# Kernel optimization log

Measured on AMD Instinct MI355X. Metric: run time of the kernel, lower is better.

Reference implementation:

```python
import jax, jax.numpy as jnp
import numpy as np

N = 100000      # nodes
E = 1600000     # edges (avg degree 16)
F_IN = 48       # input features
H = 64          # hidden
C = 2           # classes


def _init(key, shape, fan_in):
    return jax.random.normal(key, shape, jnp.float32) * (1.0 / np.sqrt(fan_in))


def setup_inputs() -> dict:
    key = jax.random.key(0)
    ks = jax.random.split(key, 12)
    return {
        "x": jax.random.normal(ks[0], (N, F_IN), jnp.float32),
        "edge_index": jax.random.randint(ks[1], (2, E), 0, N, dtype=jnp.int64),
        "W1l": _init(ks[2], (F_IN, H), F_IN),
        "b1l": jnp.zeros((H,), jnp.float32),
        "W1r": _init(ks[3], (F_IN, H), F_IN),
        "W2l": _init(ks[4], (H, H), H),
        "b2l": jnp.zeros((H,), jnp.float32),
        "W2r": _init(ks[5], (H, H), H),
        "Wlin1": _init(ks[6], (H, H), H),
        "blin1": jnp.zeros((H,), jnp.float32),
        "Wlin2": _init(ks[7], (H, C), H),
        "blin2": jnp.zeros((C,), jnp.float32),
    }


def _sage_conv(x, src, dst, Wl, bl, Wr, num_nodes):
    # mean aggregation of source-node features onto destination nodes
    msg = x[src]                                              # [E, F] gather
    agg = jax.ops.segment_sum(msg, dst, num_segments=num_nodes)
    cnt = jax.ops.segment_sum(jnp.ones((dst.shape[0], 1), x.dtype), dst,
                              num_segments=num_nodes)
    mean = agg / jnp.maximum(cnt, 1.0)
    # PyG SAGEConv: lin_l(aggr) + lin_r(root); bias only on lin_l
    return mean @ Wl + bl + x @ Wr


def reference(x, edge_index, W1l, b1l, W1r, W2l, b2l, W2r,
              Wlin1, blin1, Wlin2, blin2):
    src, dst = edge_index[0], edge_index[1]
    n = x.shape[0]
    h = jax.nn.sigmoid(_sage_conv(x, src, dst, W1l, b1l, W1r, n))
    h = jax.nn.sigmoid(_sage_conv(h, src, dst, W2l, b2l, W2r, n))
    # dropout(p=0.5) is identity in eval mode (self.training=False)
    h = jax.nn.sigmoid(h @ Wlin1 + blin1)
    return jax.nn.softmax(h @ Wlin2 + blin2, axis=1)
```

## Files before the change

### kernel.cpp

```cpp
#include <hip/hip_runtime.h>
#include <math.h>


#define NF1 48
#define HH 64
#define BKT_SHIFT 8
#define BKT_SZ (1 << BKT_SHIFT)
#define BCAP 4800
#define EPB 16

typedef __attribute__((ext_vector_type(8))) short short8v;
typedef __attribute__((ext_vector_type(4))) float float4v;

__device__ __forceinline__ float sigmoidf_(float v) {
  return 1.0f / (1.0f + __expf(-v));
}
__device__ __forceinline__ float bflo(unsigned w) {
  union { unsigned u; float f; } c; c.u = w << 16; return c.f;
}
__device__ __forceinline__ float bfhi(unsigned w) {
  union { unsigned u; float f; } c; c.u = w & 0xffff0000u; return c.f;
}
__device__ __forceinline__ unsigned short f2bf(float f) {
  union { float f; unsigned u; } c; c.f = f;
  unsigned r = c.u + 0x7fffu + ((c.u >> 16) & 1u);
  return (unsigned short)(r >> 16);
}

__global__ __launch_bounds__(256) void bin_edges(
    const int* __restrict__ ei, int* __restrict__ cursor,
    unsigned* __restrict__ bins, int E, int NB) {
  __shared__ int hist[512];
  __shared__ int gbase[512];
  for (int i = threadIdx.x; i < NB; i += 256) hist[i] = 0;
  __syncthreads();
  int base_e = blockIdx.x * (256 * EPB) + threadIdx.x;
  unsigned pk[EPB];
  int bk[EPB], rk[EPB];
#pragma unroll
  for (int k = 0; k < EPB; k++) {
    int e = base_e + k * 256;
    bk[k] = -1;
    if (e < E) {
      int s = ei[e], d = ei[E + e];
      int b = d >> BKT_SHIFT;
      pk[k] = ((unsigned)(d & (BKT_SZ - 1)) << 23) | (unsigned)s;
      bk[k] = b;
      rk[k] = atomicAdd(&hist[b], 1);
    }
  }
  __syncthreads();
  for (int i = threadIdx.x; i < NB; i += 256) {
    int c = hist[i];
    gbase[i] = (c > 0) ? atomicAdd(&cursor[i], c) : 0;
  }
  __syncthreads();
#pragma unroll
  for (int k = 0; k < EPB; k++) {
    if (bk[k] >= 0) {
      int pos = gbase[bk[k]] + rk[k];
      bins[(size_t)bk[k] * BCAP + pos] = pk[k];
    }
  }
}

__global__ __launch_bounds__(512) void scan_buckets(
    const int* __restrict__ cursor, int* __restrict__ base, int NB) {
  __shared__ int a[512], b[512];
  int tid = threadIdx.x;
  int v = (tid < NB) ? cursor[tid] : 0;
  a[tid] = v;
  __syncthreads();
  int* s = a;
  int* d = b;
  for (int off = 1; off < 512; off <<= 1) {
    int t = s[tid] + ((tid >= off) ? s[tid - off] : 0);
    d[tid] = t;
    __syncthreads();
    int* tmp = s; s = d; d = tmp;
  }
  if (tid < NB) base[tid] = s[tid] - v;
  if (tid == NB - 1) base[NB] = s[tid];
}

__global__ __launch_bounds__(256) void build_csr(
    const unsigned* __restrict__ bins, const int* __restrict__ cursor,
    const int* __restrict__ base,
    int* __restrict__ rp, int* __restrict__ csr, int n_nodes, int E, int NB) {
  __shared__ int hist[BKT_SZ];
  __shared__ int aa[BKT_SZ], bb[BKT_SZ];
  __shared__ int cur[BKT_SZ];
  int b = blockIdx.x;
  int tid = threadIdx.x;
  int node0 = b << BKT_SHIFT;
  int gb = base[b];
  int cnt = cursor[b];
  const unsigned* bp = bins + (size_t)b * BCAP;
  hist[tid] = 0;
  __syncthreads();
  for (int i = tid; i < cnt; i += 256) {
    atomicAdd(&hist[bp[i] >> 23], 1);
  }
  __syncthreads();
  int v = hist[tid];
  aa[tid] = v;
  __syncthreads();
  int* s = aa;
  int* d = bb;
  for (int off = 1; off < BKT_SZ; off <<= 1) {
    int t = s[tid] + ((tid >= off) ? s[tid - off] : 0);
    d[tid] = t;
    __syncthreads();
    int* tmp = s; s = d; d = tmp;
  }
  int loc = s[tid] - v;
  int node = node0 + tid;
  if (node < n_nodes) rp[node] = gb + loc;
  if (b == NB - 1 && tid == 0) rp[n_nodes] = E;
  cur[tid] = gb + loc;
  __syncthreads();
  for (int i = tid; i < cnt; i += 256) {
    unsigned p = bp[i];
    int dl = (int)(p >> 23);
    int pos = atomicAdd(&cur[dl], 1);
    csr[pos] = (int)(p & 0x7FFFFFu);
  }
}

template <int K>
__global__ __launch_bounds__(256, 4) void gemm_mfma(
    const float* __restrict__ X, const float* __restrict__ Wl,
    const float* __restrict__ Wr, const float* __restrict__ bias,
    unsigned short* __restrict__ t_out, float* __restrict__ r_out,
    int n_nodes) {
  __shared__ short sA[64][72];
  __shared__ short sWl[64][72];
  __shared__ short sWr[64][72];
  int lane = threadIdx.x & 63, wv = threadIdx.x >> 6;
  int l15 = lane & 15, kq = lane >> 4;

  for (int i = threadIdx.x; i < 64 * 64; i += 256) {
    int k = i >> 6, j = i & 63;
    short vl = 0, vr = 0;
    if (k < K) {
      vl = (short)f2bf(Wl[k * 64 + j]);
      vr = (short)f2bf(Wr[k * 64 + j]);
    }
    sWl[j][k] = vl;
    sWr[j][k] = vr;
  }
  if (K < 64) {
    constexpr int PADW = (64 - K) / 2;
    for (int i = threadIdx.x; i < 64 * PADW; i += 256) {
      int row = i / PADW, p = i % PADW;
      *(unsigned*)&sA[row][K + 2 * p] = 0u;
    }
  }
  float bcol[4];
#pragma unroll
  for (int c = 0; c < 4; c++) bcol[c] = bias[c * 16 + l15];

  for (int nbase = blockIdx.x * 64; nbase < n_nodes; nbase += gridDim.x * 64) {
    __syncthreads();
    for (int i = threadIdx.x; i < 64 * (K / 4); i += 256) {
      int row = i / (K / 4), c4 = i % (K / 4);
      int rr = nbase + row;
      if (rr >= n_nodes) rr = n_nodes - 1;
      float4 xv = ((const float4*)(X + (size_t)rr * K))[c4];
      unsigned lo = ((unsigned)f2bf(xv.y) << 16) | (unsigned)f2bf(xv.x);
      unsigned hi = ((unsigned)f2bf(xv.w) << 16) | (unsigned)f2bf(xv.z);
      uint2 pk = {lo, hi};
      *(uint2*)&sA[row][c4 * 4] = pk;
    }
    __syncthreads();

    float4v acc_t[4], acc_r[4];
#pragma unroll
    for (int c = 0; c < 4; c++) {
      acc_t[c] = (float4v){0.0f, 0.0f, 0.0f, 0.0f};
      acc_r[c] = (float4v){bcol[c], bcol[c], bcol[c], bcol[c]};
    }
#pragma unroll
    for (int s = 0; s < 2; s++) {
      short8v af = *(const short8v*)&sA[wv * 16 + l15][s * 32 + kq * 8];
#pragma unroll
      for (int c = 0; c < 4; c++) {
        short8v bl = *(const short8v*)&sWl[c * 16 + l15][s * 32 + kq * 8];
        short8v br = *(const short8v*)&sWr[c * 16 + l15][s * 32 + kq * 8];
        acc_t[c] = __builtin_amdgcn_mfma_f32_16x16x32_bf16(af, bl, acc_t[c], 0, 0, 0);
        acc_r[c] = __builtin_amdgcn_mfma_f32_16x16x32_bf16(af, br, acc_r[c], 0, 0, 0);
      }
    }

#pragma unroll
    for (int c = 0; c < 4; c++) {
      int j = c * 16 + l15;
#pragma unroll
      for (int g = 0; g < 4; g++) {
        int node = nbase + wv * 16 + kq * 4 + g;
        if (node < n_nodes) {
          t_out[(size_t)node * HH + j] = f2bf(acc_t[c][g]);
          r_out[(size_t)node * HH + j] = acc_r[c][g];
        }
      }
    }
  }
}

__global__ __launch_bounds__(256) void agg_sig(
    const unsigned short* __restrict__ t, const float* __restrict__ r,
    const int* __restrict__ rp, const int* __restrict__ csr,
    float* __restrict__ h, int n_nodes) {
  int grp = threadIdx.x >> 4;
  int q = threadIdx.x & 15;
  int node = blockIdx.x * 16 + grp;
  if (node >= n_nodes) return;
  int rs = rp[node], re = rp[node + 1];
  int deg = re - rs;
  const uint2* tb = (const uint2*)t + q;

  float a0 = 0, a1 = 0, a2 = 0, a3 = 0;
  int j = rs;
  for (; j + 7 < re; j += 8) {
    uint2 u0 = tb[(size_t)csr[j + 0] * 16];
    uint2 u1 = tb[(size_t)csr[j + 1] * 16];
    uint2 u2 = tb[(size_t)csr[j + 2] * 16];
    uint2 u3 = tb[(size_t)csr[j + 3] * 16];
    uint2 u4 = tb[(size_t)csr[j + 4] * 16];
    uint2 u5 = tb[(size_t)csr[j + 5] * 16];
    uint2 u6 = tb[(size_t)csr[j + 6] * 16];
    uint2 u7 = tb[(size_t)csr[j + 7] * 16];
    a0 += ((bflo(u0.x) + bflo(u1.x)) + (bflo(u2.x) + bflo(u3.x))) +
          ((bflo(u4.x) + bflo(u5.x)) + (bflo(u6.x) + bflo(u7.x)));
    a1 += ((bfhi(u0.x) + bfhi(u1.x)) + (bfhi(u2.x) + bfhi(u3.x))) +
          ((bfhi(u4.x) + bfhi(u5.x)) + (bfhi(u6.x) + bfhi(u7.x)));
    a2 += ((bflo(u0.y) + bflo(u1.y)) + (bflo(u2.y) + bflo(u3.y))) +
          ((bflo(u4.y) + bflo(u5.y)) + (bflo(u6.y) + bflo(u7.y)));
    a3 += ((bfhi(u0.y) + bfhi(u1.y)) + (bfhi(u2.y) + bfhi(u3.y))) +
          ((bfhi(u4.y) + bfhi(u5.y)) + (bfhi(u6.y) + bfhi(u7.y)));
  }
  if (j + 3 < re) {
    uint2 u0 = tb[(size_t)csr[j + 0] * 16];
    uint2 u1 = tb[(size_t)csr[j + 1] * 16];
    uint2 u2 = tb[(size_t)csr[j + 2] * 16];
    uint2 u3 = tb[(size_t)csr[j + 3] * 16];
    a0 += (bflo(u0.x) + bflo(u1.x)) + (bflo(u2.x) + bflo(u3.x));
    a1 += (bfhi(u0.x) + bfhi(u1.x)) + (bfhi(u2.x) + bfhi(u3.x));
    a2 += (bflo(u0.y) + bflo(u1.y)) + (bflo(u2.y) + bflo(u3.y));
    a3 += (bfhi(u0.y) + bfhi(u1.y)) + (bfhi(u2.y) + bfhi(u3.y));
    j += 4;
  }
  for (; j < re; j++) {
    uint2 u = tb[(size_t)csr[j] * 16];
    a0 += bflo(u.x);
    a1 += bfhi(u.x);
    a2 += bflo(u.y);
    a3 += bfhi(u.y);
  }

  float inv = 1.0f / fmaxf((float)deg, 1.0f);
  float4 rv = ((const float4*)(r + (size_t)node * HH))[q];
  float4 o;
  o.x = sigmoidf_(a0 * inv + rv.x);
  o.y = sigmoidf_(a1 * inv + rv.y);
  o.z = sigmoidf_(a2 * inv + rv.z);
  o.w = sigmoidf_(a3 * inv + rv.w);
  ((float4*)(h + (size_t)node * HH))[q] = o;
}

__global__ __launch_bounds__(512, 4) void head_k(
    const float* __restrict__ h2,
    const float* __restrict__ Wlin1, const float* __restrict__ blin1,
    const float* __restrict__ Wlin2, const float* __restrict__ blin2,
    float* __restrict__ out, int n_nodes) {
  __shared__ float sx[64][HH];
  __shared__ float sh3[64][HH];
  __shared__ float sw2[HH * 2];
  int wv = threadIdx.x >> 6, lane = threadIdx.x & 63;

  float w1[HH];
#pragma unroll
  for (int k = 0; k < HH; k++) w1[k] = Wlin1[k * HH + lane];
  float bv = blin1[lane];
  if (threadIdx.x < HH * 2) sw2[threadIdx.x] = Wlin2[threadIdx.x];
  float sb20 = blin2[0], sb21 = blin2[1];

  for (int nbase = blockIdx.x * 64; nbase < n_nodes; nbase += gridDim.x * 64) {
    __syncthreads();
    for (int i = threadIdx.x; i < 64 * (HH / 4); i += 512) {
      int row = i >> 4, c4 = i & 15;
      int rr = nbase + row;
      if (rr >= n_nodes) rr = n_nodes - 1;
      ((float4*)sx[row])[c4] = ((const float4*)(h2 + (size_t)rr * HH))[c4];
    }
    __syncthreads();

    float acc[8];
#pragma unroll
    for (int m = 0; m < 8; m++) acc[m] = bv;
#pragma unroll
    for (int k = 0; k < HH; k += 4) {
#pragma unroll
      for (int m = 0; m < 8; m++) {
        float4 a = *(const float4*)&sx[wv * 8 + m][k];
        acc[m] += a.x * w1[k] + a.y * w1[k + 1] + a.z * w1[k + 2] + a.w * w1[k + 3];
      }
    }
#pragma unroll
    for (int m = 0; m < 8; m++) sh3[wv * 8 + m][lane] = sigmoidf_(acc[m]);
    __syncthreads();

    int node_l = threadIdx.x >> 3;
    int sub = threadIdx.x & 7;
    float l0 = 0.0f, l1 = 0.0f;
#pragma unroll
    for (int kk = 0; kk < 8; kk++) {
      int k = sub * 8 + kk;
      float v = sh3[node_l][k];
      l0 += v * sw2[k * 2 + 0];
      l1 += v * sw2[k * 2 + 1];
    }
    l0 += __shfl_xor(l0, 1); l1 += __shfl_xor(l1, 1);
    l0 += __shfl_xor(l0, 2); l1 += __shfl_xor(l1, 2);
    l0 += __shfl_xor(l0, 4); l1 += __shfl_xor(l1, 4);
    int node = nbase + node_l;
    if (sub == 0 && node < n_nodes) {
      l0 += sb20;
      l1 += sb21;
      float mx = fmaxf(l0, l1);
      float p0 = __expf(l0 - mx), p1 = __expf(l1 - mx);
      float s = 1.0f / (p0 + p1);
      float2 o2 = {p0 * s, p1 * s};
      ((float2*)out)[node] = o2;
    }
  }
}

extern "C" void kernel_launch(void* const* d_in, const int* in_sizes, int n_in,
                              void* d_out, int out_size, void* d_ws, size_t ws_size,
                              hipStream_t stream) {
  const float* x     = (const float*)d_in[0];
  const int*   ei    = (const int*)d_in[1];
  const float* W1l   = (const float*)d_in[2];
  const float* b1l   = (const float*)d_in[3];
  const float* W1r   = (const float*)d_in[4];
  const float* W2l   = (const float*)d_in[5];
  const float* b2l   = (const float*)d_in[6];
  const float* W2r   = (const float*)d_in[7];
  const float* Wlin1 = (const float*)d_in[8];
  const float* blin1 = (const float*)d_in[9];
  const float* Wlin2 = (const float*)d_in[10];
  const float* blin2 = (const float*)d_in[11];
  float* out = (float*)d_out;

  int n = in_sizes[0] / NF1;
  int E = in_sizes[1] / 2;
  int NB = (n + BKT_SZ - 1) >> BKT_SHIFT;

  int* base   = (int*)d_ws;
  int* cursor = base + NB + 1;
  int* rp     = cursor + NB;
  int* csr    = rp + n + 1;
  size_t off = (size_t)(NB + 1 + NB + n + 1 + E) * sizeof(int);
  off = (off + 255) & ~(size_t)255;
  unsigned* bins = (unsigned*)((char*)d_ws + off);
  unsigned short* tbuf = (unsigned short*)bins;
  size_t reg = (size_t)NB * BCAP * sizeof(unsigned);
  size_t treg = (size_t)n * HH * sizeof(unsigned short);
  off += (reg > treg ? reg : treg);
  off = (off + 255) & ~(size_t)255;
  float* rbuf = (float*)((char*)d_ws + off);
  off += (size_t)n * HH * sizeof(float);
  off = (off + 255) & ~(size_t)255;
  float* hbuf = (float*)((char*)d_ws + off);

  hipMemsetAsync(cursor, 0, (size_t)NB * sizeof(int), stream);

  int abk = (E + 256 * EPB - 1) / (256 * EPB);
  bin_edges<<<abk, 256, 0, stream>>>(ei, cursor, bins, E, NB);
  scan_buckets<<<1, 512, 0, stream>>>(cursor, base, NB);
  build_csr<<<NB, 256, 0, stream>>>(bins, cursor, base, rp, csr, n, E, NB);

  int chunks = (n + 63) / 64;
  int gemmb = chunks < 1024 ? chunks : 1024;
  int aggb = (n + 15) / 16;
  int headb = (n + 63) / 64;
  if (headb > 1024) headb = 1024;

  gemm_mfma<NF1><<<gemmb, 256, 0, stream>>>(x, W1l, W1r, b1l, tbuf, rbuf, n);
  agg_sig<<<aggb, 256, 0, stream>>>(tbuf, rbuf, rp, csr, hbuf, n);

  gemm_mfma<HH><<<gemmb, 256, 0, stream>>>(hbuf, W2l, W2r, b2l, tbuf, rbuf, n);
  agg_sig<<<aggb, 256, 0, stream>>>(tbuf, rbuf, rp, csr, hbuf, n);

  head_k<<<headb, 512, 0, stream>>>(hbuf, Wlin1, blin1, Wlin2, blin2, out, n);
}
```

Baseline: 181.3 us.

## Fuse edge binning with first-layer GEMM and fold bucket scan into CSR build

Edge binning and the layer-1 dual GEMM now run in a single launch, with blocks split by block index, so the two independent stages overlap on the GPU. The separate single-block scan kernel is removed: each CSR-build block computes its own bucket offset by reducing the cursor counts of all earlier buckets. The bins buffer is moved into the h buffer region so it no longer aliases tbuf, which the fused GEMM writes at the same time. This saves two launches and a serial scan step, at the cost of redundant prefix sums in every CSR block and higher shared memory per block.

```diff
diff --git a/kernel.cpp b/kernel.cpp
--- a/kernel.cpp
+++ b/kernel.cpp
@@ -27,65 +27,128 @@
   return (unsigned short)(r >> 16);
 }
 
-__global__ __launch_bounds__(256) void bin_edges(
+template <int K>
+__global__ __launch_bounds__(256, 4) void fused_bin_gemm(
     const int* __restrict__ ei, int* __restrict__ cursor,
-    unsigned* __restrict__ bins, int E, int NB) {
-  __shared__ int hist[512];
-  __shared__ int gbase[512];
-  for (int i = threadIdx.x; i < NB; i += 256) hist[i] = 0;
-  __syncthreads();
-  int base_e = blockIdx.x * (256 * EPB) + threadIdx.x;
-  unsigned pk[EPB];
-  int bk[EPB], rk[EPB];
-#pragma unroll
-  for (int k = 0; k < EPB; k++) {
-    int e = base_e + k * 256;
-    bk[k] = -1;
-    if (e < E) {
-      int s = ei[e], d = ei[E + e];
-      int b = d >> BKT_SHIFT;
-      pk[k] = ((unsigned)(d & (BKT_SZ - 1)) << 23) | (unsigned)s;
-      bk[k] = b;
-      rk[k] = atomicAdd(&hist[b], 1);
-    }
-  }
-  __syncthreads();
-  for (int i = threadIdx.x; i < NB; i += 256) {
-    int c = hist[i];
-    gbase[i] = (c > 0) ? atomicAdd(&cursor[i], c) : 0;
-  }
-  __syncthreads();
-#pragma unroll
-  for (int k = 0; k < EPB; k++) {
-    if (bk[k] >= 0) {
-      int pos = gbase[bk[k]] + rk[k];
-      bins[(size_t)bk[k] * BCAP + pos] = pk[k];
-    }
-  }
-}
-
-__global__ __launch_bounds__(512) void scan_buckets(
-    const int* __restrict__ cursor, int* __restrict__ base, int NB) {
-  __shared__ int a[512], b[512];
-  int tid = threadIdx.x;
-  int v = (tid < NB) ? cursor[tid] : 0;
-  a[tid] = v;
-  __syncthreads();
-  int* s = a;
-  int* d = b;
-  for (int off = 1; off < 512; off <<= 1) {
-    int t = s[tid] + ((tid >= off) ? s[tid - off] : 0);
-    d[tid] = t;
-    __syncthreads();
-    int* tmp = s; s = d; d = tmp;
-  }
-  if (tid < NB) base[tid] = s[tid] - v;
-  if (tid == NB - 1) base[NB] = s[tid];
-}
-
-__global__ __launch_bounds__(256) void build_csr(
+    unsigned* __restrict__ bins, int E, int NB,
+    const float* __restrict__ X, const float* __restrict__ Wl,
+    const float* __restrict__ Wr, const float* __restrict__ bias,
+    unsigned short* __restrict__ t_out, float* __restrict__ r_out,
+    int n_nodes, int abk, int gemmb) {
+  __shared__ __align__(16) char smem[3 * 64 * 72 * 2];
+
+  if ((int)blockIdx.x < abk) {
+    int* hist = (int*)smem;
+    int* gbase = hist + 512;
+    for (int i = threadIdx.x; i < NB; i += 256) hist[i] = 0;
+    __syncthreads();
+    int base_e = blockIdx.x * (256 * EPB) + threadIdx.x;
+    unsigned pk[EPB];
+    int bk[EPB], rk[EPB];
+#pragma unroll
+    for (int k = 0; k < EPB; k++) {
+      int e = base_e + k * 256;
+      bk[k] = -1;
+      if (e < E) {
+        int s = ei[e], d = ei[E + e];
+        int b = d >> BKT_SHIFT;
+        pk[k] = ((unsigned)(d & (BKT_SZ - 1)) << 23) | (unsigned)s;
+        bk[k] = b;
+        rk[k] = atomicAdd(&hist[b], 1);
+      }
+    }
+    __syncthreads();
+    for (int i = threadIdx.x; i < NB; i += 256) {
+      int c = hist[i];
+      gbase[i] = (c > 0) ? atomicAdd(&cursor[i], c) : 0;
+    }
+    __syncthreads();
+#pragma unroll
+    for (int k = 0; k < EPB; k++) {
+      if (bk[k] >= 0) {
+        int pos = gbase[bk[k]] + rk[k];
+        bins[(size_t)bk[k] * BCAP + pos] = pk[k];
+      }
+    }
+    return;
+  }
+
+  short(*sA)[72] = (short(*)[72])smem;
+  short(*sWl)[72] = (short(*)[72])(smem + 9216);
+  short(*sWr)[72] = (short(*)[72])(smem + 18432);
+  int gbid = (int)blockIdx.x - abk;
+  int lane = threadIdx.x & 63, wv = threadIdx.x >> 6;
+  int l15 = lane & 15, kq = lane >> 4;
+
+  for (int i = threadIdx.x; i < 64 * 64; i += 256) {
+    int k = i >> 6, j = i & 63;
+    short vl = 0, vr = 0;
+    if (k < K) {
+      vl = (short)f2bf(Wl[k * 64 + j]);
+      vr = (short)f2bf(Wr[k * 64 + j]);
+    }
+    sWl[j][k] = vl;
+    sWr[j][k] = vr;
+  }
+  if (K < 64) {
+    constexpr int PADW = (64 - K) / 2;
+    for (int i = threadIdx.x; i < 64 * PADW; i += 256) {
+      int row = i / PADW, p = i % PADW;
+      *(unsigned*)&sA[row][K + 2 * p] = 0u;
+    }
+  }
+  float bcol[4];
+#pragma unroll
+  for (int c = 0; c < 4; c++) bcol[c] = bias[c * 16 + l15];
+
+  for (int nbase = gbid * 64; nbase < n_nodes; nbase += gemmb * 64) {
+    __syncthreads();
+    for (int i = threadIdx.x; i < 64 * (K / 4); i += 256) {
+      int row = i / (K / 4), c4 = i % (K / 4);
+      int rr = nbase + row;
+      if (rr >= n_nodes) rr = n_nodes - 1;
+      float4 xv = ((const float4*)(X + (size_t)rr * K))[c4];
+      unsigned lo = ((unsigned)f2bf(xv.y) << 16) | (unsigned)f2bf(xv.x);
+      unsigned hi = ((unsigned)f2bf(xv.w) << 16) | (unsigned)f2bf(xv.z);
+      uint2 pk2 = {lo, hi};
+      *(uint2*)&sA[row][c4 * 4] = pk2;
+    }
+    __syncthreads();
+
+    float4v acc_t[4], acc_r[4];
+#pragma unroll
+    for (int c = 0; c < 4; c++) {
+      acc_t[c] = (float4v){0.0f, 0.0f, 0.0f, 0.0f};
+      acc_r[c] = (float4v){bcol[c], bcol[c], bcol[c], bcol[c]};
+    }
+#pragma unroll
+    for (int s = 0; s < 2; s++) {
+      short8v af = *(const short8v*)&sA[wv * 16 + l15][s * 32 + kq * 8];
+#pragma unroll
+      for (int c = 0; c < 4; c++) {
+        short8v bl = *(const short8v*)&sWl[c * 16 + l15][s * 32 + kq * 8];
+        short8v br = *(const short8v*)&sWr[c * 16 + l15][s * 32 + kq * 8];
+        acc_t[c] = __builtin_amdgcn_mfma_f32_16x16x32_bf16(af, bl, acc_t[c], 0, 0, 0);
+        acc_r[c] = __builtin_amdgcn_mfma_f32_16x16x32_bf16(af, br, acc_r[c], 0, 0, 0);
+      }
+    }
+#pragma unroll
+    for (int c = 0; c < 4; c++) {
+      int j = c * 16 + l15;
+#pragma unroll
+      for (int g = 0; g < 4; g++) {
+        int node = nbase + wv * 16 + kq * 4 + g;
+        if (node < n_nodes) {
+          t_out[(size_t)node * HH + j] = f2bf(acc_t[c][g]);
+          r_out[(size_t)node * HH + j] = acc_r[c][g];
+        }
+      }
+    }
+  }
+}
+
+__global__ __launch_bounds__(256) void build_csr2(
     const unsigned* __restrict__ bins, const int* __restrict__ cursor,
-    const int* __restrict__ base,
     int* __restrict__ rp, int* __restrict__ csr, int n_nodes, int E, int NB) {
   __shared__ int hist[BKT_SZ];
   __shared__ int aa[BKT_SZ], bb[BKT_SZ];
@@ -93,9 +156,20 @@
   int b = blockIdx.x;
   int tid = threadIdx.x;
   int node0 = b << BKT_SHIFT;
-  int gb = base[b];
   int cnt = cursor[b];
   const unsigned* bp = bins + (size_t)b * BCAP;
+
+  int part = 0;
+  for (int i = tid; i < b; i += 256) part += cursor[i];
+  aa[tid] = part;
+  __syncthreads();
+  for (int off = 128; off > 0; off >>= 1) {
+    if (tid < off) aa[tid] += aa[tid + off];
+    __syncthreads();
+  }
+  int gb = aa[0];
+  __syncthreads();
+
   hist[tid] = 0;
   __syncthreads();
   for (int i = tid; i < cnt; i += 256) {
@@ -191,7 +265,6 @@
         acc_r[c] = __builtin_amdgcn_mfma_f32_16x16x32_bf16(af, br, acc_r[c], 0, 0, 0);
       }
     }
-
 #pragma unroll
     for (int c = 0; c < 4; c++) {
       int j = c * 16 + l15;
@@ -357,37 +430,34 @@
   int E = in_sizes[1] / 2;
   int NB = (n + BKT_SZ - 1) >> BKT_SHIFT;
 
-  int* base   = (int*)d_ws;
-  int* cursor = base + NB + 1;
+  int* cursor = (int*)d_ws;
   int* rp     = cursor + NB;
   int* csr    = rp + n + 1;
-  size_t off = (size_t)(NB + 1 + NB + n + 1 + E) * sizeof(int);
+  size_t off = (size_t)(NB + n + 1 + E) * sizeof(int);
   off = (off + 255) & ~(size_t)255;
-  unsigned* bins = (unsigned*)((char*)d_ws + off);
-  unsigned short* tbuf = (unsigned short*)bins;
-  size_t reg = (size_t)NB * BCAP * sizeof(unsigned);
-  size_t treg = (size_t)n * HH * sizeof(unsigned short);
-  off += (reg > treg ? reg : treg);
+  unsigned short* tbuf = (unsigned short*)((char*)d_ws + off);
+  off += (size_t)n * HH * sizeof(unsigned short);
   off = (off + 255) & ~(size_t)255;
   float* rbuf = (float*)((char*)d_ws + off);
   off += (size_t)n * HH * sizeof(float);
   off = (off + 255) & ~(size_t)255;
   float* hbuf = (float*)((char*)d_ws + off);
+  unsigned* bins = (unsigned*)hbuf;
 
   hipMemsetAsync(cursor, 0, (size_t)NB * sizeof(int), stream);
 
   int abk = (E + 256 * EPB - 1) / (256 * EPB);
-  bin_edges<<<abk, 256, 0, stream>>>(ei, cursor, bins, E, NB);
-  scan_buckets<<<1, 512, 0, stream>>>(cursor, base, NB);
-  build_csr<<<NB, 256, 0, stream>>>(bins, cursor, base, rp, csr, n, E, NB);
-
-  int chunks = (n + 63) / 64;
-  int gemmb = chunks < 1024 ? chunks : 1024;
+  int gemmb = (n + 63) / 64;
+  if (gemmb > 1024) gemmb = 1024;
   int aggb = (n + 15) / 16;
   int headb = (n + 63) / 64;
   if (headb > 1024) headb = 1024;
 
-  gemm_mfma<NF1><<<gemmb, 256, 0, stream>>>(x, W1l, W1r, b1l, tbuf, rbuf, n);
+  fused_bin_gemm<NF1><<<abk + gemmb, 256, 0, stream>>>(
+      ei, cursor, bins, E, NB, x, W1l, W1r, b1l, tbuf, rbuf, n, abk, gemmb);
+
+  build_csr2<<<NB, 256, 0, stream>>>(bins, cursor, rp, csr, n, E, NB);
+
   agg_sig<<<aggb, 256, 0, stream>>>(tbuf, rbuf, rp, csr, hbuf, n);
 
   gemm_mfma<HH><<<gemmb, 256, 0, stream>>>(hbuf, W2l, W2r, b2l, tbuf, rbuf, n);
```

Result: faster. 170.5 us (-6.0%).
